# Kernel optimization log

Hardware: AMD Instinct MI355X
Metric: run time of the kernel (lower is better)

Reference implementation:

```python
import jax, jax.numpy as jnp
import numpy as np

B, N, C, H = 8, 4096, 256, 8
D = C // H
HID = 4 * C
EPS = 1e-5

def _ln(x, w, b):
    mu = jnp.mean(x, axis=-1, keepdims=True)
    var = jnp.var(x, axis=-1, keepdims=True)
    return (x - mu) * jax.lax.rsqrt(var + EPS) * w + b

def setup_inputs() -> dict:
    key = jax.random.key(0)
    ks = jax.random.split(key, 16)
    s = lambda k, shp, scale=0.02: jax.random.normal(k, shp, dtype=jnp.float32) * scale
    return {
        "input_": jax.random.normal(ks[0], (B, N, C), dtype=jnp.float32),
        "prev_state": jax.random.normal(ks[1], (B, N, C), dtype=jnp.float32),
        "pos_embed": jax.random.normal(ks[2], (1, N, C), dtype=jnp.float32),
        "norm1_w": jnp.ones((C,), jnp.float32), "norm1_b": jnp.zeros((C,), jnp.float32),
        "norm2_w": jnp.ones((C,), jnp.float32), "norm2_b": jnp.zeros((C,), jnp.float32),
        "norm3_w": jnp.ones((C,), jnp.float32), "norm3_b": jnp.zeros((C,), jnp.float32),
        "qkv_input_w": s(ks[3], (3 * C, C)),
        "qkv_state_w": s(ks[4], (3 * C, C)),
        "proj_w": s(ks[5], (C, C)), "proj_b": jnp.zeros((C,), jnp.float32),
        "gate_w": s(ks[6], (C, 2 * C)), "gate_b": jnp.zeros((C,), jnp.float32),
        "fc1_w": s(ks[7], (HID, C)), "fc1_b": jnp.zeros((HID,), jnp.float32),
        "fc2_w": s(ks[8], (C, HID)), "fc2_b": jnp.zeros((C,), jnp.float32),
    }

def reference(input_, prev_state, pos_embed,
              norm1_w, norm1_b, norm2_w, norm2_b, norm3_w, norm3_b,
              qkv_input_w, qkv_state_w, proj_w, proj_b,
              gate_w, gate_b, fc1_w, fc1_b, fc2_w, fc2_b):
    input_pos = input_ + pos_embed
    x_ln = _ln(input_pos, norm1_w, norm1_b)
    s_ln = _ln(prev_state, norm2_w, norm2_b)
    # fused QKV from input and state; torch Linear: x @ W.T
    qkv_i = (x_ln @ qkv_input_w.T).reshape(B, N, 3, H, D).transpose(2, 0, 3, 1, 4)
    qkv_s = (s_ln @ qkv_state_w.T).reshape(B, N, 3, H, D).transpose(2, 0, 3, 1, 4)
    q = qkv_i[0] + qkv_s[0]  # [B,H,N,D]
    k = qkv_i[1] + qkv_s[1]
    v = qkv_i[2] + qkv_s[2]
    phi_q = jax.nn.elu(q) + 1.0
    phi_k = jax.nn.elu(k) + 1.0
    # (phi_q @ phi_k^T) @ v reordered associatively to O(N*D^2)
    kv = jnp.einsum('bhnd,bhne->bhde', phi_k, v)        # [B,H,D,D]
    attn = jnp.einsum('bhnd,bhde->bhne', phi_q, kv)     # [B,H,N,D]
    attn = attn.transpose(0, 2, 1, 3).reshape(B, N, C)
    attn = attn @ proj_w.T + proj_b
    output = input_pos + attn
    stacked = jnp.concatenate([input_, prev_state], axis=2)
    update = jax.nn.sigmoid(stacked @ gate_w.T + gate_b)
    new_state = prev_state * (1.0 - update) + attn * update
    h = _ln(output, norm3_w, norm3_b)
    h = jax.nn.gelu(h @ fc1_w.T + fc1_b, approximate=False) @ fc2_w.T + fc2_b
    output = output + h
    return (output, new_state)
```

## Files before the change

kernel.cpp:

```cpp
#include <hip/hip_runtime.h>
#include <cmath>

typedef unsigned short u16;
typedef __attribute__((ext_vector_type(8))) short short8;
typedef __attribute__((ext_vector_type(4))) float f32x4;
typedef __attribute__((ext_vector_type(4))) u16 u16x4;

__device__ __forceinline__ float b2f(u16 u) {
    unsigned x = ((unsigned)u) << 16;
    return __builtin_bit_cast(float, x);
}
__device__ __forceinline__ u16 f2b(float f) {
    unsigned x = __builtin_bit_cast(unsigned, f);
    unsigned r = (x + 0x7fffu + ((x >> 16) & 1u)) >> 16;
    return (u16)r;
}
__device__ __forceinline__ float loadx(const void* p, size_t i, int f32) {
    return f32 ? ((const float*)p)[i] : b2f(((const u16*)p)[i]);
}
__device__ __forceinline__ void stage8f(u16* dst, const void* src, size_t eoff) {
    const f32x4* s = (const f32x4*)((const float*)src + eoff);
    f32x4 a = s[0], b = s[1];
    uint4 p;
    p.x = (unsigned)f2b(a[0]) | ((unsigned)f2b(a[1]) << 16);
    p.y = (unsigned)f2b(a[2]) | ((unsigned)f2b(a[3]) << 16);
    p.z = (unsigned)f2b(b[0]) | ((unsigned)f2b(b[1]) << 16);
    p.w = (unsigned)f2b(b[2]) | ((unsigned)f2b(b[3]) << 16);
    *(uint4*)dst = p;
}
__device__ __forceinline__ void gl_lds16(const void* g, void* l) {
    __builtin_amdgcn_global_load_lds(
        (const __attribute__((address_space(1))) void*)g,
        (__attribute__((address_space(3))) void*)l, 16, 0, 0);
}
__device__ __forceinline__ float gelu_f(float x) {
    float y = 0.7978845608028654f * (x + 0.044715f * x * x * x);
    float e = __expf(2.f * y);
    float t = 1.f - 2.f / (e + 1.f);
    return 0.5f * x * (1.f + t);
}

#define BB 8
#define NN 4096
#define CC 256
#define HH 8
#define DD 32
#define HID 1024
#define MTOK (BB*NN)
#define TOKEL ((size_t)MTOK*CC)

#define WS_INPUT_POS 0u
#define WS_PHIQ   16777216u
#define WS_PHIK   33554432u
#define WS_V      50331648u
#define WS_XLN    67108864u
#define WS_SLN    83886080u
#define WS_OUTPRE 100663296u
#define WS_FLAG   117440512u

__global__ __launch_bounds__(64) void detect_kernel(const u16* __restrict__ in0,
                                                    int* __restrict__ flag)
{
    int t = threadIdx.x;
    u16 w = in0[2 * t];
    int e = (w >> 7) & 0xFF;
    int bad = (e < 64 || e > 192) ? 1 : 0;
    unsigned long long m = __ballot(bad);
    if (t == 0) *flag = (__popcll(m) > 8) ? 1 : 0;
}

__global__ __launch_bounds__(256) void prep_kernel(
    const void* __restrict__ inp, const void* __restrict__ prev,
    const void* __restrict__ pos,
    const void* __restrict__ w1, const void* __restrict__ b1,
    const void* __restrict__ w2, const void* __restrict__ b2,
    u16* __restrict__ input_pos, u16* __restrict__ x_ln, u16* __restrict__ s_ln,
    const int* __restrict__ flagp)
{
    const int f32 = *flagp;
    const int m = blockIdx.x;
    const int c = threadIdx.x;
    const int n = m & (NN - 1);
    const size_t idx = (size_t)m * CC + c;

    __shared__ float red[8];

    float ip = loadx(inp, idx, f32) + loadx(pos, (size_t)n * CC + c, f32);
    float s = ip, s2 = ip * ip;
    #pragma unroll
    for (int o = 32; o; o >>= 1) { s += __shfl_down(s, o, 64); s2 += __shfl_down(s2, o, 64); }
    if ((threadIdx.x & 63) == 0) { int w6 = threadIdx.x >> 6; red[w6] = s; red[4 + w6] = s2; }
    __syncthreads();
    float mu  = (red[0] + red[1] + red[2] + red[3]) * (1.f / 256.f);
    float var = (red[4] + red[5] + red[6] + red[7]) * (1.f / 256.f) - mu * mu;
    float rs = rsqrtf(var + 1e-5f);
    input_pos[idx] = f2b(ip);
    x_ln[idx] = f2b((ip - mu) * rs * loadx(w1, c, f32) + loadx(b1, c, f32));
    __syncthreads();

    float pv = loadx(prev, idx, f32);
    s = pv; s2 = pv * pv;
    #pragma unroll
    for (int o = 32; o; o >>= 1) { s += __shfl_down(s, o, 64); s2 += __shfl_down(s2, o, 64); }
    if ((threadIdx.x & 63) == 0) { int w6 = threadIdx.x >> 6; red[w6] = s; red[4 + w6] = s2; }
    __syncthreads();
    mu  = (red[0] + red[1] + red[2] + red[3]) * (1.f / 256.f);
    var = (red[4] + red[5] + red[6] + red[7]) * (1.f / 256.f) - mu * mu;
    rs = rsqrtf(var + 1e-5f);
    s_ln[idx] = f2b((pv - mu) * rs * loadx(w2, c, f32) + loadx(b2, c, f32));
}

__global__ __launch_bounds__(256) void ln3_kernel(
    const u16* __restrict__ op, const void* __restrict__ w,
    const void* __restrict__ b, u16* __restrict__ out, const int* __restrict__ flagp)
{
    const int f32 = *flagp;
    const size_t m = blockIdx.x;
    const int c = threadIdx.x;
    const size_t idx = m * CC + c;
    __shared__ float red[8];
    float x = b2f(op[idx]);
    float s = x, s2 = x * x;
    #pragma unroll
    for (int o = 32; o; o >>= 1) { s += __shfl_down(s, o, 64); s2 += __shfl_down(s2, o, 64); }
    if ((threadIdx.x & 63) == 0) { int w6 = threadIdx.x >> 6; red[w6] = s; red[4 + w6] = s2; }
    __syncthreads();
    float mu  = (red[0] + red[1] + red[2] + red[3]) * (1.f / 256.f);
    float var = (red[4] + red[5] + red[6] + red[7]) * (1.f / 256.f) - mu * mu;
    out[idx] = f2b((x - mu) * rsqrtf(var + 1e-5f) * loadx(w, c, f32) + loadx(b, c, f32));
}

__global__ __launch_bounds__(64) void kv_mfma(
    const u16* __restrict__ phik_t, const u16* __restrict__ v_t,
    float* __restrict__ kvout)
{
    const int bh = blockIdx.x;
    const int k0 = blockIdx.y * 256;
    const int lane = threadIdx.x;
    const int quad = lane >> 4, lr = lane & 15;

    const u16* A = phik_t + (size_t)bh * DD * NN;
    const u16* W = v_t    + (size_t)bh * DD * NN;

    f32x4 acc[2][2];
    #pragma unroll
    for (int i = 0; i < 2; ++i)
        #pragma unroll
        for (int j = 0; j < 2; ++j) { f32x4 z = {0.f,0.f,0.f,0.f}; acc[i][j] = z; }

    for (int kk = k0; kk < k0 + 256; kk += 32) {
        short8 a0 = *(const short8*)(A + (size_t)lr * NN + kk + quad * 8);
        short8 a1 = *(const short8*)(A + (size_t)(16 + lr) * NN + kk + quad * 8);
        short8 w0 = *(const short8*)(W + (size_t)lr * NN + kk + quad * 8);
        short8 w1 = *(const short8*)(W + (size_t)(16 + lr) * NN + kk + quad * 8);
        acc[0][0] = __builtin_amdgcn_mfma_f32_16x16x32_bf16(a0, w0, acc[0][0], 0, 0, 0);
        acc[0][1] = __builtin_amdgcn_mfma_f32_16x16x32_bf16(a0, w1, acc[0][1], 0, 0, 0);
        acc[1][0] = __builtin_amdgcn_mfma_f32_16x16x32_bf16(a1, w0, acc[1][0], 0, 0, 0);
        acc[1][1] = __builtin_amdgcn_mfma_f32_16x16x32_bf16(a1, w1, acc[1][1], 0, 0, 0);
    }
    float* base = kvout + (size_t)bh * (DD * DD);
    #pragma unroll
    for (int i = 0; i < 2; ++i)
        #pragma unroll
        for (int j = 0; j < 2; ++j)
            #pragma unroll
            for (int r = 0; r < 4; ++r)
                atomicAdd(base + (i * 16 + quad * 4 + r) * DD + j * 16 + lr, acc[i][j][r]);
}

__global__ __launch_bounds__(256) void attn_mfma(
    const u16* __restrict__ phiq, const float* __restrict__ kv,
    u16* __restrict__ attn_tok)
{
    const int bh = blockIdx.x;
    const int b = bh >> 3, h = bh & 7;
    const int wv = threadIdx.x >> 6, lane = threadIdx.x & 63;
    const int quad = lane >> 4, lr = lane & 15;

    const float* kvb = kv + (size_t)bh * (DD * DD);
    short8 bf0, bf1;
    #pragma unroll
    for (int j = 0; j < 8; ++j) {
        int d = quad * 8 + j;
        bf0[j] = (short)f2b(kvb[d * DD + lr]);
        bf1[j] = (short)f2b(kvb[d * DD + 16 + lr]);
    }

    const u16* qb = phiq + (size_t)bh * NN * DD;
    const int n0 = blockIdx.y * 512 + wv * 128;
    #pragma unroll
    for (int t = 0; t < 8; ++t) {
        const int nt = n0 + t * 16;
        short8 af = *(const short8*)(qb + (size_t)(nt + lr) * DD + quad * 8);
        f32x4 c0 = {0.f,0.f,0.f,0.f}, c1 = {0.f,0.f,0.f,0.f};
        c0 = __builtin_amdgcn_mfma_f32_16x16x32_bf16(af, bf0, c0, 0, 0, 0);
        c1 = __builtin_amdgcn_mfma_f32_16x16x32_bf16(af, bf1, c1, 0, 0, 0);
        size_t base = ((size_t)b * NN + nt + quad * 4) * CC + h * DD;
        #pragma unroll
        for (int r = 0; r < 4; ++r) {
            attn_tok[base + (size_t)r * CC + lr]      = f2b(c0[r]);
            attn_tok[base + (size_t)r * CC + 16 + lr] = f2b(c1[r]);
        }
    }
}

#define BM 128
#define BN 128
#define BK 32
#define LDT 32

template <int MODE, int RAWA>
__global__ __launch_bounds__(256) void gemm_bt(
    const void* __restrict__ A1, const void* __restrict__ A2,
    const void* __restrict__ W1, const void* __restrict__ W2,
    int lda, int ldw, int K, int Ksplit, int wcol2,
    const void* __restrict__ bias,
    u16* __restrict__ o0, u16* __restrict__ o1,
    const u16* __restrict__ xa, const void* __restrict__ xr,
    void* __restrict__ oraw, const int* __restrict__ flagp)
{
    __shared__ u16 ash[BM * LDT];
    __shared__ u16 bsh[BN * LDT];

    const int f32 = *flagp;
    const int af32 = RAWA ? f32 : 0;

    const int tid = threadIdx.x;
    const int lane = tid & 63;
    const int wv = tid >> 6;
    const int wm = wv >> 1, wn = wv & 1;
    const int quad = lane >> 4, lr = lane & 15;

    const bool swp = (MODE == 0) ? (blockIdx.x < 2) : true;

    f32x4 acc[4][4];
    #pragma unroll
    for (int i = 0; i < 4; ++i)
        #pragma unroll
        for (int j = 0; j < 4; ++j) { f32x4 z = {0.f,0.f,0.f,0.f}; acc[i][j] = z; }

    const size_t arow0 = (size_t)blockIdx.y * BM;
    const size_t wrow0 = (size_t)blockIdx.x * BN;

    const int srow = lane >> 2;
    const int skc  = (lane & 3) << 3;

    for (int k0 = 0; k0 < K; k0 += BK) {
        const void* As; const void* Ws; int ka, kw;
        if (k0 < Ksplit) { As = A1; Ws = W1; ka = k0;          kw = k0; }
        else             { As = A2; Ws = W2; ka = k0 - Ksplit; kw = k0 - Ksplit + wcol2; }

        if (!af32) {
            const u16* ga = (const u16*)As + (arow0 + wv * 32 + srow) * (size_t)lda + ka + skc;
            u16* la = ash + (wv * 32) * LDT;
            gl_lds16(ga, la);
            gl_lds16(ga + (size_t)16 * lda, la + 16 * LDT);
        } else {
            #pragma unroll
            for (int half = 0; half < 2; ++half) {
                int row = wv * 32 + half * 16 + srow;
                stage8f(ash + row * LDT + skc, As, (arow0 + row) * (size_t)lda + ka + skc);
            }
        }
        if (!f32) {
            const u16* gw = (const u16*)Ws + (wrow0 + wv * 32 + srow) * (size_t)ldw + kw + skc;
            u16* lb = bsh + (wv * 32) * LDT;
            gl_lds16(gw, lb);
            gl_lds16(gw + (size_t)16 * ldw, lb + 16 * LDT);
        } else {
            #pragma unroll
            for (int half = 0; half < 2; ++half) {
                int row = wv * 32 + half * 16 + srow;
                stage8f(bsh + row * LDT + skc, Ws, (wrow0 + row) * (size_t)ldw + kw + skc);
            }
        }
        __syncthreads();

        short8 af[4], bf[4];
        #pragma unroll
        for (int i = 0; i < 4; ++i)
            af[i] = *(const short8*)(ash + (wm * 64 + i * 16 + lr) * LDT + quad * 8);
        #pragma unroll
        for (int j = 0; j < 4; ++j)
            bf[j] = *(const short8*)(bsh + (wn * 64 + j * 16 + lr) * LDT + quad * 8);
        if (swp) {
            #pragma unroll
            for (int i = 0; i < 4; ++i)
                #pragma unroll
                for (int j = 0; j < 4; ++j)
                    acc[i][j] = __builtin_amdgcn_mfma_f32_16x16x32_bf16(bf[j], af[i], acc[i][j], 0, 0, 0);
        } else {
            #pragma unroll
            for (int i = 0; i < 4; ++i)
                #pragma unroll
                for (int j = 0; j < 4; ++j)
                    acc[i][j] = __builtin_amdgcn_mfma_f32_16x16x32_bf16(af[i], bf[j], acc[i][j], 0, 0, 0);
        }
        __syncthreads();
    }

    const int mbase = blockIdx.y * BM + wm * 64;
    const int nbase = blockIdx.x * BN + wn * 64;
    constexpr int LDOUT = (MODE == 3) ? HID : CC;

    #pragma unroll
    for (int i = 0; i < 4; ++i) {
        #pragma unroll
        for (int j = 0; j < 4; ++j) {
            if (MODE == 0) {
                if (swp) {
                    const int m = mbase + i * 16 + lr;
                    const int b = m >> 12, n = m & (NN - 1);
                    const int c0 = nbase + j * 16 + quad * 4;
                    const int h = c0 >> 5, d0 = c0 & 31;
                    u16x4 p;
                    #pragma unroll
                    for (int r = 0; r < 4; ++r) {
                        float v = acc[i][j][r];
                        p[r] = f2b((v > 0.f) ? (v + 1.f) : __expf(v));
                    }
                    *(u16x4*)(o0 + (((size_t)b * HH + h) * NN + n) * DD + d0) = p;
                } else {
                    const int c = nbase + j * 16 + lr;
                    const int which = c >> 8, rem = c & 255, h = rem >> 5, d = rem & 31;
                    const int m0 = mbase + i * 16 + quad * 4;
                    const int b = m0 >> 12, n0i = m0 & (NN - 1);
                    u16x4 p;
                    #pragma unroll
                    for (int r = 0; r < 4; ++r) {
                        float v = acc[i][j][r];
                        if (which == 1) v = (v > 0.f) ? (v + 1.f) : __expf(v);
                        p[r] = f2b(v);
                    }
                    u16* dst = o0 + (size_t)which * TOKEL;
                    *(u16x4*)(dst + (((size_t)b * HH + h) * DD + d) * NN + n0i) = p;
                }
            } else {
                const int m = mbase + i * 16 + lr;
                const int c0 = nbase + j * 16 + quad * 4;
                const size_t idx0 = (size_t)m * LDOUT + c0;
                float bias4[4];
                if (f32) {
                    f32x4 t = *(const f32x4*)((const float*)bias + c0);
                    #pragma unroll
                    for (int r = 0; r < 4; ++r) bias4[r] = t[r];
                } else {
                    u16x4 t = *(const u16x4*)((const u16*)bias + c0);
                    #pragma unroll
                    for (int r = 0; r < 4; ++r) bias4[r] = b2f(t[r]);
                }
                if (MODE == 1) {
                    u16x4 xa4 = *(const u16x4*)(xa + idx0);
                    u16x4 po, pr;
                    #pragma unroll
                    for (int r = 0; r < 4; ++r) {
                        float val = acc[i][j][r] + bias4[r];
                        po[r] = f2b(val);
                        pr[r] = f2b(b2f(xa4[r]) + val);
                    }
                    *(u16x4*)(o0 + idx0) = po;
                    *(u16x4*)(o1 + idx0) = pr;
                } else if (MODE == 2) {
                    u16x4 ap4 = *(const u16x4*)(xa + idx0);
                    float res[4];
                    if (f32) {
                        f32x4 pv = *(const f32x4*)((const float*)xr + idx0);
                        #pragma unroll
                        for (int r = 0; r < 4; ++r) {
                            float u = 1.f / (1.f + __expf(-(acc[i][j][r] + bias4[r])));
                            res[r] = pv[r] * (1.f - u) + b2f(ap4[r]) * u;
                        }
                        f32x4 o; o[0]=res[0]; o[1]=res[1]; o[2]=res[2]; o[3]=res[3];
                        *(f32x4*)((float*)oraw + TOKEL + idx0) = o;
                    } else {
                        u16x4 pv = *(const u16x4*)((const u16*)xr + idx0);
                        u16x4 o;
                        #pragma unroll
                        for (int r = 0; r < 4; ++r) {
                            float u = 1.f / (1.f + __expf(-(acc[i][j][r] + bias4[r])));
                            o[r] = f2b(b2f(pv[r]) * (1.f - u) + b2f(ap4[r]) * u);
                        }
                        *(u16x4*)((u16*)oraw + TOKEL + idx0) = o;
                    }
                } else if (MODE == 3) {
                    u16x4 p;
                    #pragma unroll
                    for (int r = 0; r < 4; ++r)
                        p[r] = f2b(gelu_f(acc[i][j][r] + bias4[r]));
                    *(u16x4*)(o0 + idx0) = p;
                } else {
                    u16x4 xa4 = *(const u16x4*)(xa + idx0);
                    if (f32) {
                        f32x4 o;
                        #pragma unroll
                        for (int r = 0; r < 4; ++r)
                            o[r] = b2f(xa4[r]) + acc[i][j][r] + bias4[r];
                        *(f32x4*)((float*)oraw + idx0) = o;
                    } else {
                        u16x4 o;
                        #pragma unroll
                        for (int r = 0; r < 4; ++r)
                            o[r] = f2b(b2f(xa4[r]) + acc[i][j][r] + bias4[r]);
                        *(u16x4*)((u16*)oraw + idx0) = o;
                    }
                }
            }
        }
    }
}

extern "C" void kernel_launch(void* const* d_in, const int* in_sizes, int n_in,
                              void* d_out, int out_size, void* d_ws, size_t ws_size,
                              hipStream_t stream)
{
    const void* input_ = d_in[0];
    const void* prev   = d_in[1];
    const void* pos    = d_in[2];
    const void* n1w = d_in[3];  const void* n1b = d_in[4];
    const void* n2w = d_in[5];  const void* n2b = d_in[6];
    const void* n3w = d_in[7];  const void* n3b = d_in[8];
    const void* qkvi = d_in[9]; const void* qkvs = d_in[10];
    const void* projw = d_in[11]; const void* projb = d_in[12];
    const void* gatew = d_in[13]; const void* gateb = d_in[14];
    const void* fc1w = d_in[15]; const void* fc1b = d_in[16];
    const void* fc2w = d_in[17]; const void* fc2b = d_in[18];

    char* ws = (char*)d_ws;
    u16* input_pos = (u16*)(ws + WS_INPUT_POS);
    u16* phiq  = (u16*)(ws + WS_PHIQ);
    u16* phikt = (u16*)(ws + WS_PHIK);
    u16* vt    = (u16*)(ws + WS_V);
    u16* x_ln = (u16*)(ws + WS_XLN);
    u16* s_ln = (u16*)(ws + WS_SLN);
    u16* attn_tok = x_ln;
    u16* attn_proj = phikt;
    float* kvf = (float*)(ws + WS_SLN);
    u16* ln3o = s_ln;
    u16* outpre = (u16*)(ws + WS_OUTPRE);
    u16* h1 = (u16*)(ws + WS_INPUT_POS);
    int* flagp = (int*)(ws + WS_FLAG);

    detect_kernel<<<1, 64, 0, stream>>>((const u16*)input_, flagp);
    prep_kernel<<<MTOK, 256, 0, stream>>>(input_, prev, pos, n1w, n1b, n2w, n2b,
                                          input_pos, x_ln, s_ln, flagp);
    gemm_bt<0, 0><<<dim3(3 * CC / BN, MTOK / BM), 256, 0, stream>>>(
        x_ln, s_ln, qkvi, qkvs, CC, CC, 2 * CC, CC, 0, nullptr,
        phiq, nullptr, nullptr, nullptr, nullptr, flagp);
    hipMemsetAsync((void*)kvf, 0, BB * HH * DD * DD * sizeof(float), stream);
    kv_mfma<<<dim3(BB * HH, 16), 64, 0, stream>>>(phikt, vt, kvf);
    attn_mfma<<<dim3(BB * HH, NN / 512), 256, 0, stream>>>(phiq, kvf, attn_tok);
    gemm_bt<1, 0><<<dim3(CC / BN, MTOK / BM), 256, 0, stream>>>(
        attn_tok, attn_tok, projw, projw, CC, CC, CC, CC, 0, projb,
        attn_proj, outpre, input_pos, nullptr, nullptr, flagp);
    gemm_bt<2, 1><<<dim3(CC / BN, MTOK / BM), 256, 0, stream>>>(
        input_, prev, gatew, gatew, CC, 2 * CC, 2 * CC, CC, CC, gateb,
        nullptr, nullptr, attn_proj, prev, d_out, flagp);
    ln3_kernel<<<MTOK, 256, 0, stream>>>(outpre, n3w, n3b, ln3o, flagp);
    gemm_bt<3, 0><<<dim3(HID / BN, MTOK / BM), 256, 0, stream>>>(
        ln3o, ln3o, fc1w, fc1w, CC, CC, CC, CC, 0, fc1b,
        h1, nullptr, nullptr, nullptr, nullptr, flagp);
    gemm_bt<4, 0><<<dim3(CC / BN, MTOK / BM), 256, 0, stream>>>(
        h1, h1, fc2w, fc2w, HID, HID, HID, HID, 0, fc2b,
        nullptr, nullptr, outpre, nullptr, d_out, flagp);
}
```

Measured before the change: 506.4 us.

## Fuse LN3, FC1+GELU and FC2 into one MLP kernel; swizzle GEMM blocks across XCDs

Replaces the separate LN3 kernel and the FC1 and FC2 GEMMs with a single mlp_kernel. Each block normalizes 64 token rows into LDS, computes the hidden activations in 128-wide chunks with GELU, and accumulates FC2 output in registers, so the 32768x1024 hidden tensor never goes to global memory. The remaining gemm_bt launches also remap block ids so that consecutive row tiles land on the same XCD, which should improve L2 locality. In exchange, the fused kernel reads FC1 and FC2 weight fragments directly from global memory with no LDS staging. Its per-block tile is small and it holds many accumulators, which may hurt MFMA efficiency and occupancy.

```diff
diff --git a/kernel.cpp b/kernel.cpp
--- a/kernel.cpp
+++ b/kernel.cpp
@@ -17,6 +17,26 @@
 }
 __device__ __forceinline__ float loadx(const void* p, size_t i, int f32) {
     return f32 ? ((const float*)p)[i] : b2f(((const u16*)p)[i]);
+}
+__device__ __forceinline__ short8 ldb8(const void* p, size_t e, int f32) {
+    if (!f32) return *(const short8*)((const u16*)p + e);
+    const float* fp = (const float*)p + e;
+    f32x4 a = *(const f32x4*)fp, b = *(const f32x4*)(fp + 4);
+    short8 r;
+    r[0] = (short)f2b(a[0]); r[1] = (short)f2b(a[1]);
+    r[2] = (short)f2b(a[2]); r[3] = (short)f2b(a[3]);
+    r[4] = (short)f2b(b[0]); r[5] = (short)f2b(b[1]);
+    r[6] = (short)f2b(b[2]); r[7] = (short)f2b(b[3]);
+    return r;
+}
+__device__ __forceinline__ f32x4 ld4f(const void* p, size_t e, int f32) {
+    f32x4 r;
+    if (f32) { r = *(const f32x4*)((const float*)p + e); }
+    else {
+        u16x4 t = *(const u16x4*)((const u16*)p + e);
+        r[0] = b2f(t[0]); r[1] = b2f(t[1]); r[2] = b2f(t[2]); r[3] = b2f(t[3]);
+    }
+    return r;
 }
 __device__ __forceinline__ void stage8f(u16* dst, const void* src, size_t eoff) {
     const f32x4* s = (const f32x4*)((const float*)src + eoff);
@@ -110,26 +130,6 @@
     s_ln[idx] = f2b((pv - mu) * rs * loadx(w2, c, f32) + loadx(b2, c, f32));
 }
 
-__global__ __launch_bounds__(256) void ln3_kernel(
-    const u16* __restrict__ op, const void* __restrict__ w,
-    const void* __restrict__ b, u16* __restrict__ out, const int* __restrict__ flagp)
-{
-    const int f32 = *flagp;
-    const size_t m = blockIdx.x;
-    const int c = threadIdx.x;
-    const size_t idx = m * CC + c;
-    __shared__ float red[8];
-    float x = b2f(op[idx]);
-    float s = x, s2 = x * x;
-    #pragma unroll
-    for (int o = 32; o; o >>= 1) { s += __shfl_down(s, o, 64); s2 += __shfl_down(s2, o, 64); }
-    if ((threadIdx.x & 63) == 0) { int w6 = threadIdx.x >> 6; red[w6] = s; red[4 + w6] = s2; }
-    __syncthreads();
-    float mu  = (red[0] + red[1] + red[2] + red[3]) * (1.f / 256.f);
-    float var = (red[4] + red[5] + red[6] + red[7]) * (1.f / 256.f) - mu * mu;
-    out[idx] = f2b((x - mu) * rsqrtf(var + 1e-5f) * loadx(w, c, f32) + loadx(b, c, f32));
-}
-
 __global__ __launch_bounds__(64) void kv_mfma(
     const u16* __restrict__ phik_t, const u16* __restrict__ v_t,
     float* __restrict__ kvout)
@@ -225,13 +225,19 @@
     const int f32 = *flagp;
     const int af32 = RAWA ? f32 : 0;
 
+    const int gx = gridDim.x, gy8 = gridDim.y >> 3;
+    int id = blockIdx.y * gx + blockIdx.x;
+    int xcd = id & 7, slot = id >> 3;
+    const int bx = slot % gx;
+    const int by = xcd * gy8 + slot / gx;
+
     const int tid = threadIdx.x;
     const int lane = tid & 63;
     const int wv = tid >> 6;
     const int wm = wv >> 1, wn = wv & 1;
     const int quad = lane >> 4, lr = lane & 15;
 
-    const bool swp = (MODE == 0) ? (blockIdx.x < 2) : true;
+    const bool swp = (MODE == 0) ? (bx < 2) : true;
 
     f32x4 acc[4][4];
     #pragma unroll
@@ -239,8 +245,8 @@
         #pragma unroll
         for (int j = 0; j < 4; ++j) { f32x4 z = {0.f,0.f,0.f,0.f}; acc[i][j] = z; }
 
-    const size_t arow0 = (size_t)blockIdx.y * BM;
-    const size_t wrow0 = (size_t)blockIdx.x * BN;
+    const size_t arow0 = (size_t)by * BM;
+    const size_t wrow0 = (size_t)bx * BN;
 
     const int srow = lane >> 2;
     const int skc  = (lane & 3) << 3;
@@ -299,9 +305,8 @@
         __syncthreads();
     }
 
-    const int mbase = blockIdx.y * BM + wm * 64;
-    const int nbase = blockIdx.x * BN + wn * 64;
-    constexpr int LDOUT = (MODE == 3) ? HID : CC;
+    const int mbase = by * BM + wm * 64;
+    const int nbase = bx * BN + wn * 64;
 
     #pragma unroll
     for (int i = 0; i < 4; ++i) {
@@ -338,17 +343,8 @@
             } else {
                 const int m = mbase + i * 16 + lr;
                 const int c0 = nbase + j * 16 + quad * 4;
-                const size_t idx0 = (size_t)m * LDOUT + c0;
-                float bias4[4];
-                if (f32) {
-                    f32x4 t = *(const f32x4*)((const float*)bias + c0);
-                    #pragma unroll
-                    for (int r = 0; r < 4; ++r) bias4[r] = t[r];
-                } else {
-                    u16x4 t = *(const u16x4*)((const u16*)bias + c0);
-                    #pragma unroll
-                    for (int r = 0; r < 4; ++r) bias4[r] = b2f(t[r]);
-                }
+                const size_t idx0 = (size_t)m * CC + c0;
+                f32x4 bias4 = ld4f(bias, c0, f32);
                 if (MODE == 1) {
                     u16x4 xa4 = *(const u16x4*)(xa + idx0);
                     u16x4 po, pr;
@@ -360,17 +356,16 @@
                     }
                     *(u16x4*)(o0 + idx0) = po;
                     *(u16x4*)(o1 + idx0) = pr;
-                } else if (MODE == 2) {
+                } else {
                     u16x4 ap4 = *(const u16x4*)(xa + idx0);
-                    float res[4];
                     if (f32) {
                         f32x4 pv = *(const f32x4*)((const float*)xr + idx0);
+                        f32x4 o;
                         #pragma unroll
                         for (int r = 0; r < 4; ++r) {
                             float u = 1.f / (1.f + __expf(-(acc[i][j][r] + bias4[r])));
-                            res[r] = pv[r] * (1.f - u) + b2f(ap4[r]) * u;
+                            o[r] = pv[r] * (1.f - u) + b2f(ap4[r]) * u;
                         }
-                        f32x4 o; o[0]=res[0]; o[1]=res[1]; o[2]=res[2]; o[3]=res[3];
                         *(f32x4*)((float*)oraw + TOKEL + idx0) = o;
                     } else {
                         u16x4 pv = *(const u16x4*)((const u16*)xr + idx0);
@@ -382,29 +377,123 @@
                         }
                         *(u16x4*)((u16*)oraw + TOKEL + idx0) = o;
                     }
-                } else if (MODE == 3) {
-                    u16x4 p;
-                    #pragma unroll
-                    for (int r = 0; r < 4; ++r)
-                        p[r] = f2b(gelu_f(acc[i][j][r] + bias4[r]));
-                    *(u16x4*)(o0 + idx0) = p;
-                } else {
-                    u16x4 xa4 = *(const u16x4*)(xa + idx0);
-                    if (f32) {
-                        f32x4 o;
-                        #pragma unroll
-                        for (int r = 0; r < 4; ++r)
-                            o[r] = b2f(xa4[r]) + acc[i][j][r] + bias4[r];
-                        *(f32x4*)((float*)oraw + idx0) = o;
-                    } else {
-                        u16x4 o;
-                        #pragma unroll
-                        for (int r = 0; r < 4; ++r)
-                            o[r] = f2b(b2f(xa4[r]) + acc[i][j][r] + bias4[r]);
-                        *(u16x4*)((u16*)oraw + idx0) = o;
-                    }
                 }
             }
+        }
+    }
+}
+
+#define MBM 64
+__global__ __launch_bounds__(256, 2) void mlp_kernel(
+    const u16* __restrict__ outpre,
+    const void* __restrict__ w3, const void* __restrict__ b3,
+    const void* __restrict__ fc1w, const void* __restrict__ fc1b,
+    const void* __restrict__ fc2w, const void* __restrict__ fc2b,
+    void* __restrict__ dout, const int* __restrict__ flagp)
+{
+    const int f32 = *flagp;
+    __shared__ u16 alds[8 * MBM * 40];
+    __shared__ u16 hlds[4 * 16 * 136];
+
+    const int tid = threadIdx.x;
+    const int wv = tid >> 6, lane = tid & 63;
+    const int quad = lane >> 4, lr = lane & 15;
+    const int row0 = blockIdx.x * MBM;
+
+    {
+        const int r4 = wv * 16 + (lane >> 2);
+        const int sub = lane & 3;
+        const u16* src = outpre + (size_t)(row0 + r4) * CC + sub * 8;
+        short8 xv[8];
+        #pragma unroll
+        for (int kt = 0; kt < 8; ++kt)
+            xv[kt] = *(const short8*)(src + kt * 32);
+        float s = 0.f, s2 = 0.f;
+        #pragma unroll
+        for (int kt = 0; kt < 8; ++kt)
+            #pragma unroll
+            for (int j = 0; j < 8; ++j) {
+                float x = b2f((u16)xv[kt][j]); s += x; s2 += x * x;
+            }
+        s += __shfl_xor(s, 1, 64);  s2 += __shfl_xor(s2, 1, 64);
+        s += __shfl_xor(s, 2, 64);  s2 += __shfl_xor(s2, 2, 64);
+        float mu = s * (1.f / 256.f);
+        float var = s2 * (1.f / 256.f) - mu * mu;
+        float rs = rsqrtf(var + 1e-5f);
+        #pragma unroll
+        for (int kt = 0; kt < 8; ++kt) {
+            int cb = kt * 32 + sub * 8;
+            short8 wv8 = ldb8(w3, cb, f32);
+            short8 bv8 = ldb8(b3, cb, f32);
+            short8 o;
+            #pragma unroll
+            for (int j = 0; j < 8; ++j) {
+                float xh = (b2f((u16)xv[kt][j]) - mu) * rs;
+                o[j] = (short)f2b(xh * b2f((u16)wv8[j]) + b2f((u16)bv8[j]));
+            }
+            *(short8*)(alds + kt * (MBM * 40) + r4 * 40 + sub * 8) = o;
+        }
+    }
+    __syncthreads();
+
+    u16* hbuf = hlds + wv * (16 * 136);
+    f32x4 oacc[16];
+    #pragma unroll
+    for (int j = 0; j < 16; ++j) { f32x4 z = {0.f,0.f,0.f,0.f}; oacc[j] = z; }
+
+    for (int hc = 0; hc < 8; ++hc) {
+        f32x4 hacc[8];
+        #pragma unroll
+        for (int j = 0; j < 8; ++j) { f32x4 z = {0.f,0.f,0.f,0.f}; hacc[j] = z; }
+        #pragma unroll
+        for (int kt = 0; kt < 8; ++kt) {
+            short8 af = *(const short8*)(alds + kt * (MBM * 40) + (wv * 16 + lr) * 40 + quad * 8);
+            #pragma unroll
+            for (int j = 0; j < 8; ++j) {
+                short8 bf = ldb8(fc1w, (size_t)(hc * 128 + j * 16 + lr) * CC + kt * 32 + quad * 8, f32);
+                hacc[j] = __builtin_amdgcn_mfma_f32_16x16x32_bf16(bf, af, hacc[j], 0, 0, 0);
+            }
+        }
+        #pragma unroll
+        for (int j = 0; j < 8; ++j) {
+            f32x4 bb = ld4f(fc1b, hc * 128 + j * 16 + quad * 4, f32);
+            u16x4 p;
+            #pragma unroll
+            for (int r = 0; r < 4; ++r)
+                p[r] = f2b(gelu_f(hacc[j][r] + bb[r]));
+            *(u16x4*)(hbuf + lr * 136 + j * 16 + quad * 4) = p;
+        }
+        __syncthreads();
+
+        #pragma unroll
+        for (int kt2 = 0; kt2 < 4; ++kt2) {
+            short8 af2 = *(const short8*)(hbuf + lr * 136 + kt2 * 32 + quad * 8);
+            #pragma unroll
+            for (int j2 = 0; j2 < 16; ++j2) {
+                short8 bf2 = ldb8(fc2w, (size_t)(j2 * 16 + lr) * HID + hc * 128 + kt2 * 32 + quad * 8, f32);
+                oacc[j2] = __builtin_amdgcn_mfma_f32_16x16x32_bf16(bf2, af2, oacc[j2], 0, 0, 0);
+            }
+        }
+        __syncthreads();
+    }
+
+    const int m = row0 + wv * 16 + lr;
+    #pragma unroll
+    for (int j2 = 0; j2 < 16; ++j2) {
+        const int c0 = j2 * 16 + quad * 4;
+        const size_t idx = (size_t)m * CC + c0;
+        f32x4 bb = ld4f(fc2b, c0, f32);
+        u16x4 xp = *(const u16x4*)(outpre + idx);
+        if (f32) {
+            f32x4 o;
+            #pragma unroll
+            for (int r = 0; r < 4; ++r) o[r] = b2f(xp[r]) + oacc[j2][r] + bb[r];
+            *(f32x4*)((float*)dout + idx) = o;
+        } else {
+            u16x4 o;
+            #pragma unroll
+            for (int r = 0; r < 4; ++r) o[r] = f2b(b2f(xp[r]) + oacc[j2][r] + bb[r]);
+            *(u16x4*)((u16*)dout + idx) = o;
         }
     }
 }
@@ -435,9 +524,7 @@
     u16* attn_tok = x_ln;
     u16* attn_proj = phikt;
     float* kvf = (float*)(ws + WS_SLN);
-    u16* ln3o = s_ln;
     u16* outpre = (u16*)(ws + WS_OUTPRE);
-    u16* h1 = (u16*)(ws + WS_INPUT_POS);
     int* flagp = (int*)(ws + WS_FLAG);
 
     detect_kernel<<<1, 64, 0, stream>>>((const u16*)input_, flagp);
@@ -455,11 +542,6 @@
     gemm_bt<2, 1><<<dim3(CC / BN, MTOK / BM), 256, 0, stream>>>(
         input_, prev, gatew, gatew, CC, 2 * CC, 2 * CC, CC, CC, gateb,
         nullptr, nullptr, attn_proj, prev, d_out, flagp);
-    ln3_kernel<<<MTOK, 256, 0, stream>>>(outpre, n3w, n3b, ln3o, flagp);
-    gemm_bt<3, 0><<<dim3(HID / BN, MTOK / BM), 256, 0, stream>>>(
-        ln3o, ln3o, fc1w, fc1w, CC, CC, CC, CC, 0, fc1b,
-        h1, nullptr, nullptr, nullptr, nullptr, flagp);
-    gemm_bt<4, 0><<<dim3(CC / BN, MTOK / BM), 256, 0, stream>>>(
-        h1, h1, fc2w, fc2w, HID, HID, HID, HID, 0, fc2b,
-        nullptr, nullptr, outpre, nullptr, d_out, flagp);
-}
+    mlp_kernel<<<MTOK / MBM, 256, 0, stream>>>(
+        outpre, n3w, n3b, fc1w, fc1b, fc2w, fc2b, d_out, flagp);
+}
```

Result: slower. 969.0 us (+91.4%).
